# Kernel optimization log

Hardware: AMD Instinct MI355X
Metric: run time of the kernel (lower is better)

The kernel has to match this reference:

```python
import jax, jax.numpy as jnp
import numpy as np

EMBED = 1024
HEADS = 16
HEAD_DIM = EMBED // HEADS


def setup_inputs() -> dict:
    key = jax.random.key(0)
    ks = jax.random.split(key, 10)
    s = 1.0 / np.sqrt(EMBED)
    inp = {
        "x": jax.random.normal(ks[0], (4, 2048, EMBED), dtype=jnp.float32),
        "mask": jax.random.randint(ks[1], (4, 2048), 0, 2, dtype=jnp.int32),
        "Wq": jax.random.uniform(ks[2], (EMBED, EMBED), jnp.float32, -s, s),
        "bq": jax.random.uniform(ks[3], (EMBED,), jnp.float32, -s, s),
        "Wk": jax.random.uniform(ks[4], (EMBED, EMBED), jnp.float32, -s, s),
        "bk": jax.random.uniform(ks[5], (EMBED,), jnp.float32, -s, s),
        "Wv": jax.random.uniform(ks[6], (EMBED, EMBED), jnp.float32, -s, s),
        "bv": jax.random.uniform(ks[7], (EMBED,), jnp.float32, -s, s),
        "Wo": jax.random.uniform(ks[8], (EMBED, EMBED), jnp.float32, -s, s),
        "bo": jax.random.uniform(ks[9], (EMBED,), jnp.float32, -s, s),
    }
    return inp


def reference(x, mask, Wq, bq, Wk, bk, Wv, bv, Wo, bo):
    B, S, E = x.shape
    scale = np.sqrt(HEAD_DIM).astype(np.float32)

    def split_heads(t):  # [B,S,E] -> [B,H,S,D]
        return t.reshape(B, S, HEADS, HEAD_DIM).transpose(0, 2, 1, 3)

    Q = split_heads(x @ Wq.T + bq)
    K = split_heads(x @ Wk.T + bk)
    V = split_heads(x @ Wv.T + bv)

    scores = jnp.einsum("bhqd,bhkd->bhqk", Q, K) / scale  # [B,H,S,S]
    # mask [B,S] broadcast over heads and query dim (key-padding mask)
    scores = jnp.where(mask[:, None, None, :] == 0, -jnp.inf, scores)
    weights = jax.nn.softmax(scores, axis=-1)
    out = jnp.einsum("bhqk,bhkd->bhqd", weights, V)  # [B,H,S,D]
    out = out.transpose(0, 2, 1, 3).reshape(B, S, E)
    return out @ Wo.T + bo
```

## Files before the change

### kernel.cpp

```cpp
#include <hip/hip_runtime.h>

#define BATCH 4
#define SEQ   2048
#define EMBED 1024
#define HEADS 16
#define HDIM  64
#define NTOK  (BATCH*SEQ)

typedef __attribute__((ext_vector_type(8)))  short short8;
typedef __attribute__((ext_vector_type(4)))  float f32x4;
typedef __attribute__((ext_vector_type(16))) float f32x16;

static __device__ __forceinline__ unsigned short f2bf(float f) {
    union { float f; unsigned u; } v; v.f = f;
    return (unsigned short)((v.u + 0x7FFFu + ((v.u >> 16) & 1u)) >> 16);
}
static __device__ __forceinline__ unsigned cvtpk(float lo, float hi) {
    unsigned r;
    asm("v_cvt_pk_bf16_f32 %0, %1, %2" : "=v"(r) : "v"(lo), "v"(hi));
    return r;
}
static __device__ __forceinline__ void gload_lds16(const unsigned short* g, unsigned short* l) {
    __builtin_amdgcn_global_load_lds(
        (__attribute__((address_space(1))) void*)g,
        (__attribute__((address_space(3))) void*)l, 16, 0, 0);
}

#define SCQ 0.180336880f

__global__ void cast_all(const float* __restrict__ x,
                         const float* __restrict__ w0, const float* __restrict__ w1,
                         const float* __restrict__ w2, const float* __restrict__ w3,
                         unsigned short* __restrict__ xb,
                         unsigned short* __restrict__ wb)
{
    const int bid = blockIdx.x;
    const float* src;
    unsigned short* dst;
    int i;
    if (bid < 4096) {
        src = x; dst = xb; i = (bid * 256 + threadIdx.x) * 8;
    } else {
        const int wz = (bid - 4096) >> 9;
        const float* ws[4] = {w0, w1, w2, w3};
        src = ws[wz];
        dst = wb + (size_t)wz * (EMBED * EMBED);
        i = (((bid - 4096) & 511) * 256 + threadIdx.x) * 8;
    }
    float4 a = *(const float4*)(src + i);
    float4 b = *(const float4*)(src + i + 4);
    union { int4 v; unsigned short u[8]; } pk;
    pk.u[0] = f2bf(a.x); pk.u[1] = f2bf(a.y); pk.u[2] = f2bf(a.z); pk.u[3] = f2bf(a.w);
    pk.u[4] = f2bf(b.x); pk.u[5] = f2bf(b.y); pk.u[6] = f2bf(b.z); pk.u[7] = f2bf(b.w);
    *(int4*)(dst + i) = pk.v;
}

__global__ __launch_bounds__(256, 2)
void gemm_qkv(const unsigned short* __restrict__ Xb,
              const unsigned short* __restrict__ Wall,
              const float* __restrict__ bq, const float* __restrict__ bk,
              const float* __restrict__ bv,
              unsigned short* __restrict__ Qw, unsigned short* __restrict__ Kw,
              unsigned short* __restrict__ VtG)
{
    __shared__ unsigned short Ws[3][128][32];
    __shared__ unsigned short Xs[128][32];

    const int tid  = threadIdx.x;
    const int bx   = blockIdx.x, by = blockIdx.y;
    const int f0   = (by >> 3) * 128;
    const int t0   = ((bx << 3) | (by & 7)) * 128;
    const int lane = tid & 63, m = lane & 15, quad = lane >> 4;
    const int wid  = tid >> 6;
    const int wf   = (wid & 1) * 64;
    const int wt   = (wid >> 1) * 64;

    const int r    = tid >> 2, cc = tid & 3, sw = (tid >> 4) & 3;
    const int gcol = (cc ^ sw) << 3;
    const unsigned short* Xp = Xb + (size_t)(t0 + r) * EMBED + gcol;
    const unsigned short* Wp = Wall + (size_t)(f0 + r) * EMBED + gcol;
    unsigned short* XsL = &Xs[0][0] + tid * 8;
    unsigned short* WsL = &Ws[0][0][0] + tid * 8;

    const int qs = (quad ^ ((m >> 2) & 3)) << 3;

    f32x4 aq[4][4] = {}, ak[4][4] = {}, av[4][4] = {};

    for (int k0 = 0; k0 < EMBED; k0 += 32) {
        __syncthreads();
        gload_lds16(Xp + k0,              XsL);
        gload_lds16(Xp + k0 + 64 * EMBED, XsL + 2048);
#pragma unroll
        for (int z = 0; z < 3; ++z) {
            const unsigned short* wz = Wp + (size_t)z * EMBED * EMBED + k0;
            gload_lds16(wz,              WsL + z * 4096);
            gload_lds16(wz + 64 * EMBED, WsL + z * 4096 + 2048);
        }
        __syncthreads();

        short8 bf4[4];
#pragma unroll
        for (int nb = 0; nb < 4; ++nb)
            bf4[nb] = *(const short8*)&Xs[wt + nb * 16 + m][qs];

#pragma unroll
        for (int z = 0; z < 3; ++z) {
            short8 af[4];
#pragma unroll
            for (int mb = 0; mb < 4; ++mb)
                af[mb] = *(const short8*)&Ws[z][wf + mb * 16 + m][qs];
            f32x4 (&acc)[4][4] = (z == 0) ? aq : (z == 1) ? ak : av;
#pragma unroll
            for (int mb = 0; mb < 4; ++mb)
#pragma unroll
                for (int nb = 0; nb < 4; ++nb)
                    acc[mb][nb] = __builtin_amdgcn_mfma_f32_16x16x32_bf16(
                        af[mb], bf4[nb], acc[mb][nb], 0, 0, 0);
        }
    }

#pragma unroll
    for (int mb = 0; mb < 4; ++mb) {
        const int feat = f0 + wf + mb * 16 + quad * 4;
        float4 bv4 = *(const float4*)&bq[feat];
#pragma unroll
        for (int nb = 0; nb < 4; ++nb) {
            const int tok = t0 + wt + nb * 16 + m;
            ushort4 pk;
            pk.x = f2bf((aq[mb][nb][0] + bv4.x) * SCQ);
            pk.y = f2bf((aq[mb][nb][1] + bv4.y) * SCQ);
            pk.z = f2bf((aq[mb][nb][2] + bv4.z) * SCQ);
            pk.w = f2bf((aq[mb][nb][3] + bv4.w) * SCQ);
            *(ushort4*)(Qw + (size_t)tok * EMBED + feat) = pk;
        }
    }
#pragma unroll
    for (int mb = 0; mb < 4; ++mb) {
        const int feat = f0 + wf + mb * 16 + quad * 4;
        float4 bv4 = *(const float4*)&bk[feat];
#pragma unroll
        for (int nb = 0; nb < 4; ++nb) {
            const int tok = t0 + wt + nb * 16 + m;
            ushort4 pk;
            pk.x = f2bf(ak[mb][nb][0] + bv4.x);
            pk.y = f2bf(ak[mb][nb][1] + bv4.y);
            pk.z = f2bf(ak[mb][nb][2] + bv4.z);
            pk.w = f2bf(ak[mb][nb][3] + bv4.w);
            *(ushort4*)(Kw + (size_t)tok * EMBED + feat) = pk;
        }
    }
    {
        const int h = (f0 + wf) >> 6;
#pragma unroll
        for (int nb = 0; nb < 4; ++nb) {
            const int tok = t0 + wt + nb * 16 + m;
            const int b   = tok >> 11;
            const int s   = tok & (SEQ - 1);
            const size_t base = ((size_t)(b * HEADS + h) * HDIM) * SEQ + s;
#pragma unroll
            for (int mb = 0; mb < 4; ++mb) {
                const int feat  = f0 + wf + mb * 16 + quad * 4;
                const int dbase = mb * 16 + quad * 4;
                float4 bv4 = *(const float4*)&bv[feat];
                VtG[base + (size_t)(dbase + 0) * SEQ] = f2bf(av[mb][nb][0] + bv4.x);
                VtG[base + (size_t)(dbase + 1) * SEQ] = f2bf(av[mb][nb][1] + bv4.y);
                VtG[base + (size_t)(dbase + 2) * SEQ] = f2bf(av[mb][nb][2] + bv4.z);
                VtG[base + (size_t)(dbase + 3) * SEQ] = f2bf(av[mb][nb][3] + bv4.w);
            }
        }
    }
}

__global__ __launch_bounds__(256, 4)
void attn_mfma(const unsigned short* __restrict__ Qb,
               const unsigned short* __restrict__ Kb,
               const unsigned short* __restrict__ VtG,
               const int* __restrict__ mask,
               unsigned short* __restrict__ Ob)
{
    __shared__ unsigned short Ks[64][72];
    __shared__ unsigned short Vs[64][72];

    const int tid  = threadIdx.x;
    const int lin  = (blockIdx.x & 7) * 128 + (blockIdx.x >> 3);
    const int qb   = lin & 15;
    const int h    = (lin >> 4) & 15;
    const int b    = lin >> 8;
    const int wid  = tid >> 6, lane = tid & 63;
    const int q32  = lane & 31, hi = lane >> 5;
    const int tb   = b * SEQ;
    const int q    = qb * 128 + wid * 32 + q32;

    const unsigned short* qrow = Qb + (size_t)(tb + q) * EMBED + h * HDIM;
    short8 qf[4];
#pragma unroll
    for (int st = 0; st < 4; ++st)
        qf[st] = *(const short8*)(qrow + st * 16 + hi * 8);

    short8 mqf = {0, 0, 0, 0, 0, 0, 0, 0};
    mqf[0] = hi ? (short)0 : (short)0xC480;

    short8 onef;
#pragma unroll
    for (int j = 0; j < 8; ++j) onef[j] = (short)0x3F80;

    f32x16 o0, o1, o2, z16;
#pragma unroll
    for (int i = 0; i < 16; ++i) { z16[i] = 0.f; }
    o0 = z16; o1 = z16; o2 = z16;

    const int sr = tid >> 2, sc = (tid & 3) * 16;
    const unsigned short* kSrc = Kb + (size_t)(tb + sr) * EMBED + h * HDIM + sc;
    const unsigned short* vSrc = VtG + ((size_t)(b * HEADS + h) * HDIM + sr) * SEQ + sc;
    const int* mrow = mask + b * SEQ;

    for (int kt = 0; kt < SEQ; kt += 64) {
        int4 kv0 = *(const int4*)(kSrc + (size_t)kt * EMBED);
        int4 kv1 = *(const int4*)(kSrc + (size_t)kt * EMBED + 8);
        int4 vv0 = *(const int4*)(vSrc + kt);
        int4 vv1 = *(const int4*)(vSrc + kt + 8);
        const int mva = mrow[kt + q32];
        const int mvb = mrow[kt + 32 + q32];
        __syncthreads();
        *(int4*)&Ks[sr][sc]     = kv0;
        *(int4*)&Ks[sr][sc + 8] = kv1;
        *(int4*)&Vs[sr][sc]     = vv0;
        *(int4*)&Vs[sr][sc + 8] = vv1;
        __syncthreads();

        short8 mkfa = {0, 0, 0, 0, 0, 0, 0, 0};
        short8 mkfb = {0, 0, 0, 0, 0, 0, 0, 0};
        mkfa[0] = (hi == 0 && mva == 0) ? (short)0x3F80 : (short)0;
        mkfb[0] = (hi == 0 && mvb == 0) ? (short)0x3F80 : (short)0;

#pragma unroll
        for (int kb = 0; kb < 2; ++kb) {
            f32x16 s = __builtin_amdgcn_mfma_f32_32x32x16_bf16(
                kb ? mkfb : mkfa, mqf, z16, 0, 0, 0);
#pragma unroll
            for (int st = 0; st < 4; ++st) {
                short8 kf = *(const short8*)&Ks[kb * 32 + q32][st * 16 + hi * 8];
                s = __builtin_amdgcn_mfma_f32_32x32x16_bf16(kf, qf[st], s, 0, 0, 0);
            }

            float p[16];
#pragma unroll
            for (int i = 0; i < 16; ++i) p[i] = __builtin_amdgcn_exp2f(s[i]);
            unsigned D[8];
#pragma unroll
            for (int j = 0; j < 8; ++j) D[j] = cvtpk(p[2 * j], p[2 * j + 1]);

#pragma unroll
            for (int cl = 0; cl < 2; ++cl) {
                unsigned x0 = D[4 * cl + 0], x1 = D[4 * cl + 1];
                unsigned x2 = D[4 * cl + 2], x3 = D[4 * cl + 3];
                asm("v_permlane32_swap_b32 %0, %1" : "+v"(x0), "+v"(x2));
                asm("v_permlane32_swap_b32 %0, %1" : "+v"(x1), "+v"(x3));
                union { uint4 u; short8 s8; } fr;
                fr.u.x = x0; fr.u.y = x1; fr.u.z = x2; fr.u.w = x3;

                const int kcol = kb * 32 + cl * 16 + hi * 8;
                short8 vf0 = *(const short8*)&Vs[q32][kcol];
                short8 vf1 = *(const short8*)&Vs[32 + q32][kcol];
                o0 = __builtin_amdgcn_mfma_f32_32x32x16_bf16(vf0, fr.s8, o0, 0, 0, 0);
                o1 = __builtin_amdgcn_mfma_f32_32x32x16_bf16(vf1, fr.s8, o1, 0, 0, 0);
                o2 = __builtin_amdgcn_mfma_f32_32x32x16_bf16(onef, fr.s8, o2, 0, 0, 0);
            }
        }
    }

    const float inv = 1.0f / o2[0];
    unsigned short* orow = Ob + (size_t)(tb + q) * EMBED + h * HDIM;
#pragma unroll
    for (int db = 0; db < 2; ++db) {
        const f32x16& oo = db ? o1 : o0;
#pragma unroll
        for (int qg = 0; qg < 4; ++qg) {
            ushort4 pk;
            pk.x = f2bf(oo[qg * 4 + 0] * inv);
            pk.y = f2bf(oo[qg * 4 + 1] * inv);
            pk.z = f2bf(oo[qg * 4 + 2] * inv);
            pk.w = f2bf(oo[qg * 4 + 3] * inv);
            *(ushort4*)(orow + db * 32 + qg * 8 + hi * 4) = pk;
        }
    }
}

__global__ __launch_bounds__(256, 2)
void gemm_o(const unsigned short* __restrict__ W, const unsigned short* __restrict__ X,
            const float* __restrict__ bias, float* __restrict__ Cout)
{
    __shared__ unsigned short Ws[128][32];
    __shared__ unsigned short Xs[128][32];

    const int tid  = threadIdx.x;
    const int bx   = blockIdx.x, by = blockIdx.y;
    const int f0   = (by >> 3) * 128;
    const int t0   = ((bx << 3) | (by & 7)) * 128;
    const int lane = tid & 63, m = lane & 15, quad = lane >> 4;
    const int wid  = tid >> 6;
    const int wf   = (wid & 1) * 64;
    const int wt   = (wid >> 1) * 64;

    const int r    = tid >> 2, cc = tid & 3, sw = (tid >> 4) & 3;
    const int gcol = (cc ^ sw) << 3;
    const unsigned short* Wp = W + (size_t)(f0 + r) * EMBED + gcol;
    const unsigned short* Xp = X + (size_t)(t0 + r) * EMBED + gcol;
    unsigned short* WsL = &Ws[0][0] + tid * 8;
    unsigned short* XsL = &Xs[0][0] + tid * 8;

    const int qs = (quad ^ ((m >> 2) & 3)) << 3;

    f32x4 acc[4][4] = {};

    for (int k0 = 0; k0 < EMBED; k0 += 32) {
        __syncthreads();
        gload_lds16(Wp + k0,              WsL);
        gload_lds16(Wp + k0 + 64 * EMBED, WsL + 2048);
        gload_lds16(Xp + k0,              XsL);
        gload_lds16(Xp + k0 + 64 * EMBED, XsL + 2048);
        __syncthreads();

        short8 af[4], bf4[4];
#pragma unroll
        for (int mb = 0; mb < 4; ++mb)
            af[mb] = *(const short8*)&Ws[wf + mb * 16 + m][qs];
#pragma unroll
        for (int nb = 0; nb < 4; ++nb)
            bf4[nb] = *(const short8*)&Xs[wt + nb * 16 + m][qs];
#pragma unroll
        for (int mb = 0; mb < 4; ++mb)
#pragma unroll
            for (int nb = 0; nb < 4; ++nb)
                acc[mb][nb] = __builtin_amdgcn_mfma_f32_16x16x32_bf16(
                    af[mb], bf4[nb], acc[mb][nb], 0, 0, 0);
    }

#pragma unroll
    for (int mb = 0; mb < 4; ++mb) {
        const int feat = f0 + wf + mb * 16 + quad * 4;
        float4 bv4 = *(const float4*)&bias[feat];
#pragma unroll
        for (int nb = 0; nb < 4; ++nb) {
            const int tok = t0 + wt + nb * 16 + m;
            float4 st;
            st.x = acc[mb][nb][0] + bv4.x;
            st.y = acc[mb][nb][1] + bv4.y;
            st.z = acc[mb][nb][2] + bv4.z;
            st.w = acc[mb][nb][3] + bv4.w;
            *(float4*)(Cout + (size_t)tok * EMBED + feat) = st;
        }
    }
}

extern "C" void kernel_launch(void* const* d_in, const int* in_sizes, int n_in,
                              void* d_out, int out_size, void* d_ws, size_t ws_size,
                              hipStream_t stream)
{
    const float* x    = (const float*)d_in[0];
    const int*   mask = (const int*)  d_in[1];
    const float* Wq   = (const float*)d_in[2];
    const float* bq   = (const float*)d_in[3];
    const float* Wk   = (const float*)d_in[4];
    const float* bk   = (const float*)d_in[5];
    const float* Wv   = (const float*)d_in[6];
    const float* bv   = (const float*)d_in[7];
    const float* Wo   = (const float*)d_in[8];
    const float* bo   = (const float*)d_in[9];
    float* out = (float*)d_out;

    const size_t NE = (size_t)NTOK * EMBED;
    const size_t WE = (size_t)EMBED * EMBED;
    unsigned short* Xb  = (unsigned short*)d_ws;
    unsigned short* Wqb = Xb + NE;
    unsigned short* Wob = Wqb + 3 * WE;
    unsigned short* Qw  = Wob + WE;
    unsigned short* Kw  = Qw + NE;
    unsigned short* VtG = Kw + NE;
    unsigned short* Ow  = Xb;

    cast_all<<<4096 + 2048, 256, 0, stream>>>(x, Wq, Wk, Wv, Wo, Xb, Wqb);

    gemm_qkv<<<dim3(8, 64), 256, 0, stream>>>(Xb, Wqb, bq, bk, bv, Qw, Kw, VtG);

    attn_mfma<<<BATCH * HEADS * (SEQ / 128), 256, 0, stream>>>(Qw, Kw, VtG, mask, Ow);

    gemm_o<<<dim3(8, 64), 256, 0, stream>>>(Wob, Ow, bo, out);
}
```

Before: 272.9 us.

## Double attention KV tile to 128 keys and precompute key mask as bitmask

```diff
diff --git a/kernel.cpp b/kernel.cpp
--- a/kernel.cpp
+++ b/kernel.cpp
@@ -178,8 +178,8 @@
                const int* __restrict__ mask,
                unsigned short* __restrict__ Ob)
 {
-    __shared__ unsigned short Ks[64][72];
-    __shared__ unsigned short Vs[64][72];
+    __shared__ unsigned short Ks[128][72];
+    __shared__ unsigned short Vs[64][136];
 
     const int tid  = threadIdx.x;
     const int lin  = (blockIdx.x & 7) * 128 + (blockIdx.x >> 3);
@@ -197,6 +197,12 @@
     for (int st = 0; st < 4; ++st)
         qf[st] = *(const short8*)(qrow + st * 16 + hi * 8);
 
+    const int* mrow = mask + b * SEQ;
+    unsigned long long mbits = 0;
+#pragma unroll 8
+    for (int j = 0; j < 64; ++j)
+        mbits |= (unsigned long long)(mrow[j * 32 + q32] != 0 ? 1 : 0) << j;
+
     short8 mqf = {0, 0, 0, 0, 0, 0, 0, 0};
     mqf[0] = hi ? (short)0 : (short)0xC480;
 
@@ -209,34 +215,44 @@
     for (int i = 0; i < 16; ++i) { z16[i] = 0.f; }
     o0 = z16; o1 = z16; o2 = z16;
 
-    const int sr = tid >> 2, sc = (tid & 3) * 16;
-    const unsigned short* kSrc = Kb + (size_t)(tb + sr) * EMBED + h * HDIM + sc;
-    const unsigned short* vSrc = VtG + ((size_t)(b * HEADS + h) * HDIM + sr) * SEQ + sc;
-    const int* mrow = mask + b * SEQ;
-
-    for (int kt = 0; kt < SEQ; kt += 64) {
-        int4 kv0 = *(const int4*)(kSrc + (size_t)kt * EMBED);
-        int4 kv1 = *(const int4*)(kSrc + (size_t)kt * EMBED + 8);
+    const int kr = tid >> 1, kc = (tid & 1) * 32;
+    const int vr = tid >> 2, vc = (tid & 3) * 32;
+    const unsigned short* kSrc = Kb + (size_t)(tb + kr) * EMBED + h * HDIM + kc;
+    const unsigned short* vSrc = VtG + ((size_t)(b * HEADS + h) * HDIM + vr) * SEQ + vc;
+
+    for (int kt = 0; kt < SEQ; kt += 128) {
+        const unsigned short* kp = kSrc + (size_t)kt * EMBED;
+        int4 kv0 = *(const int4*)(kp);
+        int4 kv1 = *(const int4*)(kp + 8);
+        int4 kv2 = *(const int4*)(kp + 16);
+        int4 kv3 = *(const int4*)(kp + 24);
         int4 vv0 = *(const int4*)(vSrc + kt);
         int4 vv1 = *(const int4*)(vSrc + kt + 8);
-        const int mva = mrow[kt + q32];
-        const int mvb = mrow[kt + 32 + q32];
-        __syncthreads();
-        *(int4*)&Ks[sr][sc]     = kv0;
-        *(int4*)&Ks[sr][sc + 8] = kv1;
-        *(int4*)&Vs[sr][sc]     = vv0;
-        *(int4*)&Vs[sr][sc + 8] = vv1;
-        __syncthreads();
-
-        short8 mkfa = {0, 0, 0, 0, 0, 0, 0, 0};
-        short8 mkfb = {0, 0, 0, 0, 0, 0, 0, 0};
-        mkfa[0] = (hi == 0 && mva == 0) ? (short)0x3F80 : (short)0;
-        mkfb[0] = (hi == 0 && mvb == 0) ? (short)0x3F80 : (short)0;
-
-#pragma unroll
-        for (int kb = 0; kb < 2; ++kb) {
+        int4 vv2 = *(const int4*)(vSrc + kt + 16);
+        int4 vv3 = *(const int4*)(vSrc + kt + 24);
+        __syncthreads();
+        *(int4*)&Ks[kr][kc]      = kv0;
+        *(int4*)&Ks[kr][kc + 8]  = kv1;
+        *(int4*)&Ks[kr][kc + 16] = kv2;
+        *(int4*)&Ks[kr][kc + 24] = kv3;
+        *(int4*)&Vs[vr][vc]      = vv0;
+        *(int4*)&Vs[vr][vc + 8]  = vv1;
+        *(int4*)&Vs[vr][vc + 16] = vv2;
+        *(int4*)&Vs[vr][vc + 24] = vv3;
+        __syncthreads();
+
+        const int jb = kt >> 5;
+        short8 mkf[4] = {{0,0,0,0,0,0,0,0},{0,0,0,0,0,0,0,0},
+                         {0,0,0,0,0,0,0,0},{0,0,0,0,0,0,0,0}};
+#pragma unroll
+        for (int kb = 0; kb < 4; ++kb)
+            mkf[kb][0] = (hi == 0 && !((mbits >> (jb + kb)) & 1))
+                         ? (short)0x3F80 : (short)0;
+
+#pragma unroll
+        for (int kb = 0; kb < 4; ++kb) {
             f32x16 s = __builtin_amdgcn_mfma_f32_32x32x16_bf16(
-                kb ? mkfb : mkfa, mqf, z16, 0, 0, 0);
+                mkf[kb], mqf, z16, 0, 0, 0);
 #pragma unroll
             for (int st = 0; st < 4; ++st) {
                 short8 kf = *(const short8*)&Ks[kb * 32 + q32][st * 16 + hi * 8];
```

Result: no change. 277.9 us (+1.8%).

## Process two query tiles per wave in attention to reuse K/V fragments

Applied to the files above, without the earlier changes.

```diff
diff --git a/kernel.cpp b/kernel.cpp
--- a/kernel.cpp
+++ b/kernel.cpp
@@ -171,7 +171,7 @@
     }
 }
 
-__global__ __launch_bounds__(256, 4)
+__global__ __launch_bounds__(128, 2)
 void attn_mfma(const unsigned short* __restrict__ Qb,
                const unsigned short* __restrict__ Kb,
                const unsigned short* __restrict__ VtG,
@@ -189,13 +189,16 @@
     const int wid  = tid >> 6, lane = tid & 63;
     const int q32  = lane & 31, hi = lane >> 5;
     const int tb   = b * SEQ;
-    const int q    = qb * 128 + wid * 32 + q32;
-
-    const unsigned short* qrow = Qb + (size_t)(tb + q) * EMBED + h * HDIM;
-    short8 qf[4];
-#pragma unroll
-    for (int st = 0; st < 4; ++st)
-        qf[st] = *(const short8*)(qrow + st * 16 + hi * 8);
+    const int q0   = qb * 128 + wid * 64 + q32;
+
+    short8 qf[2][4];
+#pragma unroll
+    for (int t = 0; t < 2; ++t) {
+        const unsigned short* qrow = Qb + (size_t)(tb + q0 + t * 32) * EMBED + h * HDIM;
+#pragma unroll
+        for (int st = 0; st < 4; ++st)
+            qf[t][st] = *(const short8*)(qrow + st * 16 + hi * 8);
+    }
 
     short8 mqf = {0, 0, 0, 0, 0, 0, 0, 0};
     mqf[0] = hi ? (short)0 : (short)0xC480;
@@ -204,28 +207,38 @@
 #pragma unroll
     for (int j = 0; j < 8; ++j) onef[j] = (short)0x3F80;
 
-    f32x16 o0, o1, o2, z16;
+    f32x16 o00, o01, o02, o10, o11, o12, z16;
 #pragma unroll
     for (int i = 0; i < 16; ++i) { z16[i] = 0.f; }
-    o0 = z16; o1 = z16; o2 = z16;
-
-    const int sr = tid >> 2, sc = (tid & 3) * 16;
+    o00 = z16; o01 = z16; o02 = z16;
+    o10 = z16; o11 = z16; o12 = z16;
+
+    const int sr = tid >> 1, sc = (tid & 1) * 32;
     const unsigned short* kSrc = Kb + (size_t)(tb + sr) * EMBED + h * HDIM + sc;
     const unsigned short* vSrc = VtG + ((size_t)(b * HEADS + h) * HDIM + sr) * SEQ + sc;
     const int* mrow = mask + b * SEQ;
 
     for (int kt = 0; kt < SEQ; kt += 64) {
-        int4 kv0 = *(const int4*)(kSrc + (size_t)kt * EMBED);
-        int4 kv1 = *(const int4*)(kSrc + (size_t)kt * EMBED + 8);
+        const unsigned short* kp = kSrc + (size_t)kt * EMBED;
+        int4 kv0 = *(const int4*)(kp);
+        int4 kv1 = *(const int4*)(kp + 8);
+        int4 kv2 = *(const int4*)(kp + 16);
+        int4 kv3 = *(const int4*)(kp + 24);
         int4 vv0 = *(const int4*)(vSrc + kt);
         int4 vv1 = *(const int4*)(vSrc + kt + 8);
+        int4 vv2 = *(const int4*)(vSrc + kt + 16);
+        int4 vv3 = *(const int4*)(vSrc + kt + 24);
         const int mva = mrow[kt + q32];
         const int mvb = mrow[kt + 32 + q32];
         __syncthreads();
-        *(int4*)&Ks[sr][sc]     = kv0;
-        *(int4*)&Ks[sr][sc + 8] = kv1;
-        *(int4*)&Vs[sr][sc]     = vv0;
-        *(int4*)&Vs[sr][sc + 8] = vv1;
+        *(int4*)&Ks[sr][sc]      = kv0;
+        *(int4*)&Ks[sr][sc + 8]  = kv1;
+        *(int4*)&Ks[sr][sc + 16] = kv2;
+        *(int4*)&Ks[sr][sc + 24] = kv3;
+        *(int4*)&Vs[sr][sc]      = vv0;
+        *(int4*)&Vs[sr][sc + 8]  = vv1;
+        *(int4*)&Vs[sr][sc + 16] = vv2;
+        *(int4*)&Vs[sr][sc + 24] = vv3;
         __syncthreads();
 
         short8 mkfa = {0, 0, 0, 0, 0, 0, 0, 0};
@@ -235,53 +248,76 @@
 
 #pragma unroll
         for (int kb = 0; kb < 2; ++kb) {
-            f32x16 s = __builtin_amdgcn_mfma_f32_32x32x16_bf16(
+            f32x16 seed = __builtin_amdgcn_mfma_f32_32x32x16_bf16(
                 kb ? mkfb : mkfa, mqf, z16, 0, 0, 0);
+            short8 kf[4];
+#pragma unroll
+            for (int st = 0; st < 4; ++st)
+                kf[st] = *(const short8*)&Ks[kb * 32 + q32][st * 16 + hi * 8];
+
+            f32x16 s0 = seed, s1 = seed;
 #pragma unroll
             for (int st = 0; st < 4; ++st) {
-                short8 kf = *(const short8*)&Ks[kb * 32 + q32][st * 16 + hi * 8];
-                s = __builtin_amdgcn_mfma_f32_32x32x16_bf16(kf, qf[st], s, 0, 0, 0);
+                s0 = __builtin_amdgcn_mfma_f32_32x32x16_bf16(kf[st], qf[0][st], s0, 0, 0, 0);
+                s1 = __builtin_amdgcn_mfma_f32_32x32x16_bf16(kf[st], qf[1][st], s1, 0, 0, 0);
             }
 
             float p[16];
-#pragma unroll
-            for (int i = 0; i < 16; ++i) p[i] = __builtin_amdgcn_exp2f(s[i]);
-            unsigned D[8];
-#pragma unroll
-            for (int j = 0; j < 8; ++j) D[j] = cvtpk(p[2 * j], p[2 * j + 1]);
+            unsigned D0[8], D1[8];
+#pragma unroll
+            for (int i = 0; i < 16; ++i) p[i] = __builtin_amdgcn_exp2f(s0[i]);
+#pragma unroll
+            for (int j = 0; j < 8; ++j) D0[j] = cvtpk(p[2 * j], p[2 * j + 1]);
+#pragma unroll
+            for (int i = 0; i < 16; ++i) p[i] = __builtin_amdgcn_exp2f(s1[i]);
+#pragma unroll
+            for (int j = 0; j < 8; ++j) D1[j] = cvtpk(p[2 * j], p[2 * j + 1]);
 
 #pragma unroll
             for (int cl = 0; cl < 2; ++cl) {
-                unsigned x0 = D[4 * cl + 0], x1 = D[4 * cl + 1];
-                unsigned x2 = D[4 * cl + 2], x3 = D[4 * cl + 3];
-                asm("v_permlane32_swap_b32 %0, %1" : "+v"(x0), "+v"(x2));
-                asm("v_permlane32_swap_b32 %0, %1" : "+v"(x1), "+v"(x3));
-                union { uint4 u; short8 s8; } fr;
-                fr.u.x = x0; fr.u.y = x1; fr.u.z = x2; fr.u.w = x3;
+                unsigned a0 = D0[4 * cl + 0], a1 = D0[4 * cl + 1];
+                unsigned a2 = D0[4 * cl + 2], a3 = D0[4 * cl + 3];
+                asm("v_permlane32_swap_b32 %0, %1" : "+v"(a0), "+v"(a2));
+                asm("v_permlane32_swap_b32 %0, %1" : "+v"(a1), "+v"(a3));
+                union { uint4 u; short8 s8; } fr0;
+                fr0.u.x = a0; fr0.u.y = a1; fr0.u.z = a2; fr0.u.w = a3;
+
+                unsigned b0 = D1[4 * cl + 0], b1 = D1[4 * cl + 1];
+                unsigned b2 = D1[4 * cl + 2], b3 = D1[4 * cl + 3];
+                asm("v_permlane32_swap_b32 %0, %1" : "+v"(b0), "+v"(b2));
+                asm("v_permlane32_swap_b32 %0, %1" : "+v"(b1), "+v"(b3));
+                union { uint4 u; short8 s8; } fr1;
+                fr1.u.x = b0; fr1.u.y = b1; fr1.u.z = b2; fr1.u.w = b3;
 
                 const int kcol = kb * 32 + cl * 16 + hi * 8;
                 short8 vf0 = *(const short8*)&Vs[q32][kcol];
                 short8 vf1 = *(const short8*)&Vs[32 + q32][kcol];
-                o0 = __builtin_amdgcn_mfma_f32_32x32x16_bf16(vf0, fr.s8, o0, 0, 0, 0);
-                o1 = __builtin_amdgcn_mfma_f32_32x32x16_bf16(vf1, fr.s8, o1, 0, 0, 0);
-                o2 = __builtin_amdgcn_mfma_f32_32x32x16_bf16(onef, fr.s8, o2, 0, 0, 0);
+                o00 = __builtin_amdgcn_mfma_f32_32x32x16_bf16(vf0, fr0.s8, o00, 0, 0, 0);
+                o01 = __builtin_amdgcn_mfma_f32_32x32x16_bf16(vf1, fr0.s8, o01, 0, 0, 0);
+                o02 = __builtin_amdgcn_mfma_f32_32x32x16_bf16(onef, fr0.s8, o02, 0, 0, 0);
+                o10 = __builtin_amdgcn_mfma_f32_32x32x16_bf16(vf0, fr1.s8, o10, 0, 0, 0);
+                o11 = __builtin_amdgcn_mfma_f32_32x32x16_bf16(vf1, fr1.s8, o11, 0, 0, 0);
+                o12 = __builtin_amdgcn_mfma_f32_32x32x16_bf16(onef, fr1.s8, o12, 0, 0, 0);
             }
         }
     }
 
-    const float inv = 1.0f / o2[0];
-    unsigned short* orow = Ob + (size_t)(tb + q) * EMBED + h * HDIM;
-#pragma unroll
-    for (int db = 0; db < 2; ++db) {
-        const f32x16& oo = db ? o1 : o0;
-#pragma unroll
-        for (int qg = 0; qg < 4; ++qg) {
-            ushort4 pk;
-            pk.x = f2bf(oo[qg * 4 + 0] * inv);
-            pk.y = f2bf(oo[qg * 4 + 1] * inv);
-            pk.z = f2bf(oo[qg * 4 + 2] * inv);
-            pk.w = f2bf(oo[qg * 4 + 3] * inv);
-            *(ushort4*)(orow + db * 32 + qg * 8 + hi * 4) = pk;
+#pragma unroll
+    for (int t = 0; t < 2; ++t) {
+        const float inv = 1.0f / (t ? o12[0] : o02[0]);
+        unsigned short* orow = Ob + (size_t)(tb + q0 + t * 32) * EMBED + h * HDIM;
+#pragma unroll
+        for (int db = 0; db < 2; ++db) {
+            const f32x16& oo = t ? (db ? o11 : o10) : (db ? o01 : o00);
+#pragma unroll
+            for (int qg = 0; qg < 4; ++qg) {
+                ushort4 pk;
+                pk.x = f2bf(oo[qg * 4 + 0] * inv);
+                pk.y = f2bf(oo[qg * 4 + 1] * inv);
+                pk.z = f2bf(oo[qg * 4 + 2] * inv);
+                pk.w = f2bf(oo[qg * 4 + 3] * inv);
+                *(ushort4*)(orow + db * 32 + qg * 8 + hi * 4) = pk;
+            }
         }
     }
 }
@@ -383,7 +419,7 @@
 
     gemm_qkv<<<dim3(8, 64), 256, 0, stream>>>(Xb, Wqb, bq, bk, bv, Qw, Kw, VtG);
 
-    attn_mfma<<<BATCH * HEADS * (SEQ / 128), 256, 0, stream>>>(Qw, Kw, VtG, mask, Ow);
+    attn_mfma<<<BATCH * HEADS * (SEQ / 128), 128, 0, stream>>>(Qw, Kw, VtG, mask, Ow);
 
     gemm_o<<<dim3(8, 64), 256, 0, stream>>>(Wob, Ow, bo, out);
 }
```

New measurement: 271.6 us. About the same (-0.5%).

## Double-buffer K/V tiles in attention and compute row sums on VALU

Applied to the files above, without the earlier changes.

```diff
diff --git a/kernel.cpp b/kernel.cpp
--- a/kernel.cpp
+++ b/kernel.cpp
@@ -178,8 +178,8 @@
                const int* __restrict__ mask,
                unsigned short* __restrict__ Ob)
 {
-    __shared__ unsigned short Ks[64][72];
-    __shared__ unsigned short Vs[64][72];
+    __shared__ unsigned short Ks[2][64][72];
+    __shared__ unsigned short Vs[2][64][72];
 
     const int tid  = threadIdx.x;
     const int lin  = (blockIdx.x & 7) * 128 + (blockIdx.x >> 3);
@@ -200,52 +200,41 @@
     short8 mqf = {0, 0, 0, 0, 0, 0, 0, 0};
     mqf[0] = hi ? (short)0 : (short)0xC480;
 
-    short8 onef;
-#pragma unroll
-    for (int j = 0; j < 8; ++j) onef[j] = (short)0x3F80;
-
-    f32x16 o0, o1, o2, z16;
+    f32x16 o0, o1, z16;
 #pragma unroll
     for (int i = 0; i < 16; ++i) { z16[i] = 0.f; }
-    o0 = z16; o1 = z16; o2 = z16;
+    o0 = z16; o1 = z16;
+    float lr = 0.f;
 
     const int sr = tid >> 2, sc = (tid & 3) * 16;
     const unsigned short* kSrc = Kb + (size_t)(tb + sr) * EMBED + h * HDIM + sc;
     const unsigned short* vSrc = VtG + ((size_t)(b * HEADS + h) * HDIM + sr) * SEQ + sc;
     const int* mrow = mask + b * SEQ;
 
-    for (int kt = 0; kt < SEQ; kt += 64) {
-        int4 kv0 = *(const int4*)(kSrc + (size_t)kt * EMBED);
-        int4 kv1 = *(const int4*)(kSrc + (size_t)kt * EMBED + 8);
-        int4 vv0 = *(const int4*)(vSrc + kt);
-        int4 vv1 = *(const int4*)(vSrc + kt + 8);
-        const int mva = mrow[kt + q32];
-        const int mvb = mrow[kt + 32 + q32];
-        __syncthreads();
-        *(int4*)&Ks[sr][sc]     = kv0;
-        *(int4*)&Ks[sr][sc + 8] = kv1;
-        *(int4*)&Vs[sr][sc]     = vv0;
-        *(int4*)&Vs[sr][sc + 8] = vv1;
-        __syncthreads();
-
+    auto compute = [&](const unsigned short (*Kc)[72],
+                       const unsigned short (*Vc)[72], int mva, int mvb) {
+        __builtin_amdgcn_s_setprio(1);
         short8 mkfa = {0, 0, 0, 0, 0, 0, 0, 0};
         short8 mkfb = {0, 0, 0, 0, 0, 0, 0, 0};
         mkfa[0] = (hi == 0 && mva == 0) ? (short)0x3F80 : (short)0;
         mkfb[0] = (hi == 0 && mvb == 0) ? (short)0x3F80 : (short)0;
-
 #pragma unroll
         for (int kb = 0; kb < 2; ++kb) {
             f32x16 s = __builtin_amdgcn_mfma_f32_32x32x16_bf16(
                 kb ? mkfb : mkfa, mqf, z16, 0, 0, 0);
 #pragma unroll
             for (int st = 0; st < 4; ++st) {
-                short8 kf = *(const short8*)&Ks[kb * 32 + q32][st * 16 + hi * 8];
+                short8 kf = *(const short8*)&Kc[kb * 32 + q32][st * 16 + hi * 8];
                 s = __builtin_amdgcn_mfma_f32_32x32x16_bf16(kf, qf[st], s, 0, 0, 0);
             }
 
             float p[16];
 #pragma unroll
             for (int i = 0; i < 16; ++i) p[i] = __builtin_amdgcn_exp2f(s[i]);
+
+            lr += (((p[0] + p[1]) + (p[2] + p[3])) + ((p[4] + p[5]) + (p[6] + p[7])))
+                + (((p[8] + p[9]) + (p[10] + p[11])) + ((p[12] + p[13]) + (p[14] + p[15])));
+
             unsigned D[8];
 #pragma unroll
             for (int j = 0; j < 8; ++j) D[j] = cvtpk(p[2 * j], p[2 * j + 1]);
@@ -260,16 +249,55 @@
                 fr.u.x = x0; fr.u.y = x1; fr.u.z = x2; fr.u.w = x3;
 
                 const int kcol = kb * 32 + cl * 16 + hi * 8;
-                short8 vf0 = *(const short8*)&Vs[q32][kcol];
-                short8 vf1 = *(const short8*)&Vs[32 + q32][kcol];
+                short8 vf0 = *(const short8*)&Vc[q32][kcol];
+                short8 vf1 = *(const short8*)&Vc[32 + q32][kcol];
                 o0 = __builtin_amdgcn_mfma_f32_32x32x16_bf16(vf0, fr.s8, o0, 0, 0, 0);
                 o1 = __builtin_amdgcn_mfma_f32_32x32x16_bf16(vf1, fr.s8, o1, 0, 0, 0);
-                o2 = __builtin_amdgcn_mfma_f32_32x32x16_bf16(onef, fr.s8, o2, 0, 0, 0);
             }
         }
-    }
-
-    const float inv = 1.0f / o2[0];
+        __builtin_amdgcn_s_setprio(0);
+    };
+
+    int mva_c, mvb_c;
+    {
+        int4 kv0 = *(const int4*)(kSrc);
+        int4 kv1 = *(const int4*)(kSrc + 8);
+        int4 vv0 = *(const int4*)(vSrc);
+        int4 vv1 = *(const int4*)(vSrc + 8);
+        mva_c = mrow[q32];
+        mvb_c = mrow[32 + q32];
+        *(int4*)&Ks[0][sr][sc]     = kv0;
+        *(int4*)&Ks[0][sr][sc + 8] = kv1;
+        *(int4*)&Vs[0][sr][sc]     = vv0;
+        *(int4*)&Vs[0][sr][sc + 8] = vv1;
+        __syncthreads();
+    }
+
+    int cur = 0;
+    for (int kt = 0; kt + 64 < SEQ; kt += 64) {
+        const unsigned short* kp = kSrc + (size_t)(kt + 64) * EMBED;
+        int4 kv0 = *(const int4*)(kp);
+        int4 kv1 = *(const int4*)(kp + 8);
+        int4 vv0 = *(const int4*)(vSrc + kt + 64);
+        int4 vv1 = *(const int4*)(vSrc + kt + 64 + 8);
+        const int mva_n = mrow[kt + 64 + q32];
+        const int mvb_n = mrow[kt + 96 + q32];
+
+        compute(Ks[cur], Vs[cur], mva_c, mvb_c);
+
+        __syncthreads();
+        const int nxt = cur ^ 1;
+        *(int4*)&Ks[nxt][sr][sc]     = kv0;
+        *(int4*)&Ks[nxt][sr][sc + 8] = kv1;
+        *(int4*)&Vs[nxt][sr][sc]     = vv0;
+        *(int4*)&Vs[nxt][sr][sc + 8] = vv1;
+        __syncthreads();
+        mva_c = mva_n; mvb_c = mvb_n; cur = nxt;
+    }
+    compute(Ks[cur], Vs[cur], mva_c, mvb_c);
+
+    const float lrt = lr + __shfl_xor(lr, 32);
+    const float inv = 1.0f / lrt;
     unsigned short* orow = Ob + (size_t)(tb + q) * EMBED + h * HDIM;
 #pragma unroll
     for (int db = 0; db < 2; ++db) {
```

Result: no change. 276.2 us (+1.2%).
